# Performance work log

Hardware: AMD Instinct MI355X
Metric: run time of the kernel (lower is better)

## Reference

```python
import jax, jax.numpy as jnp
import numpy as np

B, D, N, H = 1024, 1024, 51, 10
NUM_ITERS = 5
BN_EPS = 1e-3  # Keras BatchNormalization default epsilon


def setup_inputs():
    key = jax.random.key(0)
    ks = jax.random.split(key, 20)
    rn = lambda k, sh, s=0.05: jax.random.normal(k, sh, dtype=jnp.float32) * s
    z = lambda sh: jnp.zeros(sh, jnp.float32)
    o = lambda sh: jnp.ones(sh, jnp.float32)
    return {
        "nonvis_vec": rn(ks[0], (B, 2 * D), 1.0),
        "featuremap": rn(ks[1], (B, H, H, D), 1.0),
        "prior": rn(ks[2], (B, N), 1.0),
        "W1": rn(ks[3], (3 * D, 2 * D)), "b1": z((2 * D,)),
        "g1": o((2 * D,)), "be1": z((2 * D,)), "m1": rn(ks[4], (2 * D,)), "v1": o((2 * D,)),
        "W2": rn(ks[5], (2 * D, D)), "b2": z((D,)),
        "g2": o((D,)), "be2": z((D,)), "m2": rn(ks[6], (D,)), "v2": o((D,)),
        "Wk": rn(ks[7], (D, 3 * D)), "Uk": rn(ks[8], (D, 3 * D)),
        "bi": z((3 * D,)), "br": z((3 * D,)),
        "ct1_w": rn(ks[9], (3, 3, D, D // 4)), "ct1_b": z((D // 4,)),
        "ct2_w": rn(ks[10], (3, 3, D // 4, D // 16)), "ct2_b": z((D // 16,)),
        "ct3_w": rn(ks[11], (3, 3, D // 16, D // 64)), "ct3_b": z((D // 64,)),
        "ct4_w": rn(ks[12], (3, 3, D // 64, 1)), "ct4_b": z((1,)),
        "Ws": rn(ks[13], (3 * D, N)), "bs": z((N,)),
    }


def _bn(x, g, be, m, v):
    # inference-mode batchnorm (moving statistics)
    return (x - m) * jax.lax.rsqrt(v + BN_EPS) * g + be


def _gru_step(x, h, Wk, Uk, bi, br):
    # Keras GRU, reset_after=True, single timestep
    mx = x @ Wk + bi          # [B, 3D]
    mi = h @ Uk + br          # [B, 3D]
    xz, xr, xh = jnp.split(mx, 3, axis=-1)
    iz, ir, ih = jnp.split(mi, 3, axis=-1)
    zg = jax.nn.sigmoid(xz + iz)
    rg = jax.nn.sigmoid(xr + ir)
    hh = jnp.tanh(xh + rg * ih)
    return zg * h + (1.0 - zg) * hh


def _convT(x, w, b):
    return jax.lax.conv_transpose(x, w, (2, 2), 'SAME',
                                  dimension_numbers=('NHWC', 'HWIO', 'NHWC')) + b


def _attention(h, ct1_w, ct1_b, ct2_w, ct2_b, ct3_w, ct3_b, ct4_w, ct4_b):
    b = h.shape[0]
    a = h[:, None, None, :]                                  # [B,1,1,D]
    a = jax.nn.relu(_convT(a, ct1_w, ct1_b))                 # [B,2,2,D/4]
    a = jax.nn.relu(_convT(a, ct2_w, ct2_b))                 # [B,4,4,D/16]
    a = jax.nn.relu(_convT(a, ct3_w, ct3_b))                 # [B,8,8,D/64]
    a = _convT(a, ct4_w, ct4_b)                              # [B,16,16,1]
    a = jax.image.resize(a, (b, H, H, 1), method='bilinear')  # [B,10,10,1]
    # joint softmax over both spatial axes
    a = jax.nn.softmax(a.reshape(b, H * H, 1), axis=1).reshape(b, H, H, 1)
    return a


def reference(nonvis_vec, featuremap, prior, W1, b1, g1, be1, m1, v1,
              W2, b2, g2, be2, m2, v2, Wk, Uk, bi, br,
              ct1_w, ct1_b, ct2_w, ct2_b, ct3_w, ct3_b, ct4_w, ct4_b, Ws, bs):
    vis_vec = jnp.mean(featuremap, axis=(1, 2))              # GlobalAvgPool2D
    combined = jnp.concatenate([nonvis_vec, vis_vec], axis=-1)
    score = combined @ Ws + bs
    h = jnp.zeros((combined.shape[0], D), combined.dtype)
    for _ in range(NUM_ITERS):
        x = _bn(jax.nn.relu(combined @ W1 + b1), g1, be1, m1, v1)
        x = _bn(jax.nn.relu(x @ W2 + b2), g2, be2, m2, v2)
        h = _gru_step(x, h, Wk, Uk, bi, br)
        attn = _attention(h, ct1_w, ct1_b, ct2_w, ct2_b, ct3_w, ct3_b, ct4_w, ct4_b)
        vis_vec = jnp.sum(featuremap * attn, axis=(1, 2))    # attention pooling
        combined = jnp.concatenate([nonvis_vec, vis_vec], axis=-1)
        score = score + combined @ Ws + bs
    score = score / (NUM_ITERS + 1)
    return score + prior
```

## Files before the change

### kernel.cpp

```cpp
#include <hip/hip_runtime.h>

typedef unsigned short u16;
typedef __attribute__((ext_vector_type(8))) __bf16 bf16x8;
typedef __attribute__((ext_vector_type(4))) float f32x4;

typedef __attribute__((address_space(1))) const void gvoid_t;
typedef __attribute__((address_space(3))) void lvoid_t;

enum { E_CADD = 1, E_BIAS = 2, E_RELU = 4, E_AFF = 8, E_WBF = 16, E_WF32 = 32 };

static __device__ __forceinline__ u16 f2bf(float f) {
  unsigned u = __float_as_uint(f);
  u += 0x7fffu + ((u >> 16) & 1u);
  return (u16)(u >> 16);
}
static __device__ __forceinline__ float bf2f(u16 h) {
  return __uint_as_float(((unsigned)h) << 16);
}

template <int FLAGS>
static __device__ __forceinline__ void gemm64_body(
    u16* As, u16* Bs,
    const u16* __restrict__ A, const u16* __restrict__ Bt,
    float* __restrict__ Cf, u16* __restrict__ Cb,
    const float* __restrict__ Cadd, const float* __restrict__ bias,
    const float* __restrict__ scale, const float* __restrict__ shift,
    int N, int K, int bx, int by) {
  const int tid = threadIdx.x;
  const int wave = tid >> 6, lane = tid & 63;
  const int bm = by << 6, bn = bx << 6;
  const int wm = (wave >> 1) << 5, wn = (wave & 1) << 5;
  const int lr = lane & 15, lg = lane >> 4;
  const int rx = lr & 7;

  f32x4 acc[2][2] = {};

  for (int kt = 0; kt < K; kt += 64) {
#pragma unroll
    for (int i = 0; i < 2; ++i) {
      const int li = i * 256 + tid;
      const int row = li >> 3;
      const int cg = (li & 7) ^ (row & 7);
      const int lb = (i * 256 + wave * 64) * 8;
      __builtin_amdgcn_global_load_lds(
          (gvoid_t*)(A + (size_t)(bm + row) * K + kt + (cg << 3)),
          (lvoid_t*)(As + lb), 16, 0, 0);
      __builtin_amdgcn_global_load_lds(
          (gvoid_t*)(Bt + (size_t)(bn + row) * K + kt + (cg << 3)),
          (lvoid_t*)(Bs + lb), 16, 0, 0);
    }
    __syncthreads();
#pragma unroll
    for (int kk = 0; kk < 64; kk += 32) {
      bf16x8 av[2], bv[2];
#pragma unroll
      for (int mi = 0; mi < 2; ++mi)
        av[mi] = *(const bf16x8*)(As + ((wm + mi * 16 + lr) << 6) +
                                  ((((kk >> 3) + lg) ^ rx) << 3));
#pragma unroll
      for (int ni = 0; ni < 2; ++ni)
        bv[ni] = *(const bf16x8*)(Bs + ((wn + ni * 16 + lr) << 6) +
                                  ((((kk >> 3) + lg) ^ rx) << 3));
#pragma unroll
      for (int mi = 0; mi < 2; ++mi)
#pragma unroll
        for (int ni = 0; ni < 2; ++ni)
          acc[mi][ni] = __builtin_amdgcn_mfma_f32_16x16x32_bf16(av[mi], bv[ni], acc[mi][ni], 0, 0, 0);
    }
    __syncthreads();
  }

#pragma unroll
  for (int mi = 0; mi < 2; ++mi) {
#pragma unroll
    for (int ni = 0; ni < 2; ++ni) {
      const int col = bn + wn + ni * 16 + lr;
#pragma unroll
      for (int r = 0; r < 4; ++r) {
        const int row = bm + wm + mi * 16 + (lg << 2) + r;
        float v = acc[mi][ni][r];
        if (FLAGS & E_CADD) v += Cadd[(size_t)row * N + col];
        if (FLAGS & E_BIAS) v += bias[col];
        if (FLAGS & E_RELU) v = fmaxf(v, 0.f);
        if (FLAGS & E_AFF) v = v * scale[col] + shift[col];
        if (FLAGS & E_WF32) Cf[(size_t)row * N + col] = v;
        if (FLAGS & E_WBF) Cb[(size_t)row * N + col] = f2bf(v);
      }
    }
  }
}

template <int FLAGS>
__global__ __launch_bounds__(256) void gemm64_k(
    const u16* __restrict__ A, const u16* __restrict__ Bt,
    float* __restrict__ Cf, u16* __restrict__ Cb,
    const float* __restrict__ Cadd, const float* __restrict__ bias,
    const float* __restrict__ scale, const float* __restrict__ shift,
    int N, int K) {
  __shared__ u16 As[4096], Bs[4096];
  gemm64_body<FLAGS>(As, Bs, A, Bt, Cf, Cb, Cadd, bias, scale, shift, N, K,
                     blockIdx.x, blockIdx.y);
}

template <int F0, int F1>
__global__ __launch_bounds__(256) void gemm64_pair_k(
    const u16* A0, const u16* B0, float* Cf0, u16* Cb0, const float* Cadd0,
    const float* bias0, const float* scale0, const float* shift0, int N0, int K0, int xt0,
    const u16* A1, const u16* B1, float* Cf1, u16* Cb1, const float* Cadd1,
    const float* bias1, const float* scale1, const float* shift1, int N1, int K1, int xt1) {
  __shared__ u16 As[4096], Bs[4096];
  if (blockIdx.z == 0) {
    if ((int)blockIdx.x < xt0)
      gemm64_body<F0>(As, Bs, A0, B0, Cf0, Cb0, Cadd0, bias0, scale0, shift0,
                      N0, K0, blockIdx.x, blockIdx.y);
  } else {
    if ((int)blockIdx.x < xt1)
      gemm64_body<F1>(As, Bs, A1, B1, Cf1, Cb1, Cadd1, bias1, scale1, shift1,
                      N1, K1, blockIdx.x, blockIdx.y);
  }
}

__global__ __launch_bounds__(256) void prep_w_k(
    const float* __restrict__ W1, const float* __restrict__ W2,
    const float* __restrict__ Wk, const float* __restrict__ Uk,
    const float* __restrict__ Ws,
    u16* __restrict__ W1nv_t, u16* __restrict__ W1v_t, u16* __restrict__ W2t,
    u16* __restrict__ Wkt, u16* __restrict__ Ukt,
    u16* __restrict__ Wsnv_t, u16* __restrict__ Wsv_t) {
  int b = blockIdx.x;
  const float* in; u16* out; int ld, k0, K, Nv, kT;
  if (b < 1024)      {           in = W1; out = W1nv_t; ld = 2048; k0 = 0;    K = 2048; Nv = 2048; kT = 32; }
  else if (b < 1536) { b -= 1024; in = W1; out = W1v_t;  ld = 2048; k0 = 2048; K = 1024; Nv = 2048; kT = 16; }
  else if (b < 2048) { b -= 1536; in = W2; out = W2t;   ld = 1024; k0 = 0;    K = 2048; Nv = 1024; kT = 32; }
  else if (b < 2816) { b -= 2048; in = Wk; out = Wkt;   ld = 3072; k0 = 0;    K = 1024; Nv = 3072; kT = 16; }
  else if (b < 3584) { b -= 2816; in = Uk; out = Ukt;   ld = 3072; k0 = 0;    K = 1024; Nv = 3072; kT = 16; }
  else if (b < 3648) { b -= 3584; in = Ws; out = Wsnv_t; ld = 51;  k0 = 0;    K = 2048; Nv = 51;   kT = 32; }
  else               { b -= 3648; in = Ws; out = Wsv_t;  ld = 51;  k0 = 2048; K = 1024; Nv = 51;   kT = 16; }
  const int kt = (b % kT) << 6, nt = (b / kT) << 6;
  __shared__ float t[64][65];
  const int tx = threadIdx.x & 63, ty = threadIdx.x >> 6;
#pragma unroll
  for (int i = 0; i < 16; ++i) {
    const int kl = ty + i * 4;
    const int n = nt + tx;
    t[kl][tx] = (n < Nv) ? in[(size_t)(k0 + kt + kl) * ld + n] : 0.f;
  }
  __syncthreads();
#pragma unroll
  for (int i = 0; i < 16; ++i)
    out[(size_t)(nt + ty + i * 4) * K + kt + tx] = f2bf(t[tx][ty + i * 4]);
}

__global__ void build_all_k(
    const float* __restrict__ w1, const float* __restrict__ b1c,
    const float* __restrict__ w2, const float* __restrict__ b2c,
    const float* __restrict__ w3, const float* __restrict__ b3c,
    const float* __restrict__ w4, const float* __restrict__ b4c,
    u16* __restrict__ Wp1, u16* __restrict__ Wp2,
    u16* __restrict__ Wp3, u16* __restrict__ Wp4,
    float* __restrict__ bp1, float* __restrict__ bp2,
    float* __restrict__ bp3, float* __restrict__ bp4) {
  int y = blockIdx.y;
  const float* w; const float* bin; u16* wp; float* bp; int Si, CI, CO, n;
  if (y < 1024)      { n = y;        w = w1; bin = b1c; wp = Wp1; bp = bp1; Si = 1; CI = 1024; CO = 256; }
  else if (y < 2048) { n = y - 1024; w = w2; bin = b2c; wp = Wp2; bp = bp2; Si = 2; CI = 256;  CO = 64; }
  else if (y < 3072) { n = y - 2048; w = w3; bin = b3c; wp = Wp3; bp = bp3; Si = 4; CI = 64;   CO = 16; }
  else               { n = y - 3072; w = w4; bin = b4c; wp = Wp4; bp = bp4; Si = 8; CI = 16;   CO = 1; }
  const int So = Si * 2;
  const int K = Si * Si * CI;
  const int k = blockIdx.x * 256 + threadIdx.x;
  const int co = n % CO;
  const int pox = (n / CO) % So;
  const int poy = n / (CO * So);
  const int ci = k % CI;
  const int pix = (k / CI) % Si;
  const int piy = k / (CI * Si);
  int wy = -1, wx = -1;
  if (poy & 1) { if (piy == (poy >> 1)) wy = 1; }
  else { if (piy == (poy >> 1)) wy = 2; else if (piy == (poy >> 1) - 1) wy = 0; }
  if (pox & 1) { if (pix == (pox >> 1)) wx = 1; }
  else { if (pix == (pox >> 1)) wx = 2; else if (pix == (pox >> 1) - 1) wx = 0; }
  float v = 0.f;
  if (wy >= 0 && wx >= 0) v = w[((size_t)(wy * 3 + wx) * CI + ci) * CO + co];
  wp[(size_t)n * K + k] = f2bf(v);
  if (k == 0) bp[n] = bin[co];
}

__global__ __launch_bounds__(256) void fm_pass_k(
    const float* __restrict__ fm, u16* __restrict__ fmb,
    float* __restrict__ vis_sum, u16* __restrict__ visb, int wfmb) {
  const int b = blockIdx.x;
  const int d0 = threadIdx.x << 2;
  const float* p = fm + (size_t)b * 102400 + d0;
  float s0 = 0, s1 = 0, s2 = 0, s3 = 0;
  for (int pp = 0; pp < 100; ++pp) {
    const float4 v = *(const float4*)(p + pp * 1024);
    if (wfmb) {
      ushort4 u;
      u.x = f2bf(v.x); u.y = f2bf(v.y); u.z = f2bf(v.z); u.w = f2bf(v.w);
      *(ushort4*)(fmb + (size_t)b * 102400 + pp * 1024 + d0) = u;
    }
    s0 += v.x; s1 += v.y; s2 += v.z; s3 += v.w;
  }
  const float inv = 1.0f / 100.0f;
  s0 *= inv; s1 *= inv; s2 *= inv; s3 *= inv;
  const int o = (b << 10) + d0;
  float4 m; m.x = s0; m.y = s1; m.z = s2; m.w = s3;
  *(float4*)(vis_sum + o) = m;
  ushort4 u; u.x = f2bf(s0); u.y = f2bf(s1); u.z = f2bf(s2); u.w = f2bf(s3);
  *(ushort4*)(visb + o) = u;
}

__global__ __launch_bounds__(256) void misc_k(
    const float* __restrict__ nonvis, u16* __restrict__ nonvis_b,
    const float* g1, const float* be1, const float* m1, const float* v1,
    const float* g2, const float* be2, const float* m2, const float* v2,
    const float* bs, float* scale1, float* shift1, float* scale2, float* shift2,
    float* bs_pad, float* __restrict__ hf, u16* __restrict__ hb) {
  const int i = blockIdx.x * 256 + threadIdx.x;
  if (i < 2097152) nonvis_b[i] = f2bf(nonvis[i]);
  if (i < 1048576) { hf[i] = 0.f; hb[i] = 0; }
  if (i < 2048) { float sc = g1[i] * rsqrtf(v1[i] + 1e-3f); scale1[i] = sc; shift1[i] = be1[i] - m1[i] * sc; }
  if (i < 1024) { float sc = g2[i] * rsqrtf(v2[i] + 1e-3f); scale2[i] = sc; shift2[i] = be2[i] - m2[i] * sc; }
  if (i < 128) bs_pad[i] = (i < 51) ? bs[i] : 0.f;
}

__global__ __launch_bounds__(256) void gru_k(const float* __restrict__ mx, const float* __restrict__ mi,
                                             float* __restrict__ hf, u16* __restrict__ hb) {
  const int idx = blockIdx.x * 256 + threadIdx.x;
  const int b = idx >> 10, d = idx & 1023;
  const float* mxb = mx + (size_t)b * 3072;
  const float* mib = mi + (size_t)b * 3072;
  const float xz = mxb[d], xr = mxb[d + 1024], xh = mxb[d + 2048];
  const float iz = mib[d], ir = mib[d + 1024], ih = mib[d + 2048];
  const float zg = 1.f / (1.f + expf(-(xz + iz)));
  const float rg = 1.f / (1.f + expf(-(xr + ir)));
  const float hh = tanhf(xh + rg * ih);
  const float hn = zg * hf[idx] + (1.f - zg) * hh;
  hf[idx] = hn;
  hb[idx] = f2bf(hn);
}

static __device__ __forceinline__ void taps(int o, int& si, float* w) {
  const float s = 1.6f * (float)o + 0.3f;
  int s0 = (int)ceilf(s - 1.6f);
  if (s0 < 0) s0 = 0;
  si = s0;
  float sum = 0.f;
#pragma unroll
  for (int j = 0; j < 4; ++j) {
    const int i = s0 + j;
    float ww = 0.f;
    if (i <= 15) {
      const float d = fabsf(s - (float)i) * (1.0f / 1.6f);
      ww = fmaxf(0.f, 1.f - d);
    }
    w[j] = ww;
    sum += ww;
  }
  const float inv = 1.f / sum;
#pragma unroll
  for (int j = 0; j < 4; ++j) w[j] *= inv;
}

__global__ __launch_bounds__(128) void attn_k(const float* __restrict__ a4, float* __restrict__ attn) {
  const int b = blockIdx.x, t = threadIdx.x;
  __shared__ float sm[128];
  float val = -1e30f;
  if (t < 100) {
    const int oy = t / 10, ox = t - oy * 10;
    int siy, six;
    float wy[4], wx[4];
    taps(oy, siy, wy);
    taps(ox, six, wx);
    const float* p = a4 + (b << 8);
    float s = 0.f;
#pragma unroll
    for (int jy = 0; jy < 4; ++jy) {
      const int iy = min(siy + jy, 15);
      float rs = 0.f;
#pragma unroll
      for (int jx = 0; jx < 4; ++jx) {
        const int ix = min(six + jx, 15);
        rs += wx[jx] * p[(iy << 4) + ix];
      }
      s += wy[jy] * rs;
    }
    val = s;
  }
  sm[t] = val;
  __syncthreads();
  for (int off = 64; off > 0; off >>= 1) {
    if (t < off) sm[t] = fmaxf(sm[t], sm[t + off]);
    __syncthreads();
  }
  const float mx = sm[0];
  __syncthreads();
  const float e = (t < 100) ? expf(val - mx) : 0.f;
  sm[t] = e;
  __syncthreads();
  for (int off = 64; off > 0; off >>= 1) {
    if (t < off) sm[t] += sm[t + off];
    __syncthreads();
  }
  if (t < 100) attn[b * 100 + t] = e / sm[0];
}

__global__ __launch_bounds__(256) void wsum_bf16_k(const u16* __restrict__ fmb,
                                                   const float* __restrict__ attn,
                                                   float* __restrict__ vis_sum,
                                                   u16* __restrict__ visb,
                                                   u16* __restrict__ vsb) {
  const int b = blockIdx.x;
  __shared__ float at[100];
  if (threadIdx.x < 100) at[threadIdx.x] = attn[b * 100 + threadIdx.x];
  __syncthreads();
  const int d0 = threadIdx.x << 2;
  const u16* p = fmb + (size_t)b * 102400 + d0;
  float s0 = 0, s1 = 0, s2 = 0, s3 = 0;
  for (int pp = 0; pp < 100; ++pp) {
    const ushort4 v = *(const ushort4*)(p + pp * 1024);
    const float a = at[pp];
    s0 += a * bf2f(v.x); s1 += a * bf2f(v.y); s2 += a * bf2f(v.z); s3 += a * bf2f(v.w);
  }
  const int o = (b << 10) + d0;
  float4 vs = *(float4*)(vis_sum + o);
  vs.x += s0; vs.y += s1; vs.z += s2; vs.w += s3;
  *(float4*)(vis_sum + o) = vs;
  ushort4 u; u.x = f2bf(s0); u.y = f2bf(s1); u.z = f2bf(s2); u.w = f2bf(s3);
  *(ushort4*)(visb + o) = u;
  ushort4 w; w.x = f2bf(vs.x); w.y = f2bf(vs.y); w.z = f2bf(vs.z); w.w = f2bf(vs.w);
  *(ushort4*)(vsb + o) = w;
}

__global__ __launch_bounds__(256) void wsum_f32_k(const float* __restrict__ fm,
                                                  const float* __restrict__ attn,
                                                  float* __restrict__ vis_sum,
                                                  u16* __restrict__ visb,
                                                  u16* __restrict__ vsb) {
  const int b = blockIdx.x;
  __shared__ float at[100];
  if (threadIdx.x < 100) at[threadIdx.x] = attn[b * 100 + threadIdx.x];
  __syncthreads();
  const int d0 = threadIdx.x << 2;
  const float* p = fm + (size_t)b * 102400 + d0;
  float s0 = 0, s1 = 0, s2 = 0, s3 = 0;
  for (int pp = 0; pp < 100; ++pp) {
    const float4 v = *(const float4*)(p + pp * 1024);
    const float a = at[pp];
    s0 += a * v.x; s1 += a * v.y; s2 += a * v.z; s3 += a * v.w;
  }
  const int o = (b << 10) + d0;
  float4 vs = *(float4*)(vis_sum + o);
  vs.x += s0; vs.y += s1; vs.z += s2; vs.w += s3;
  *(float4*)(vis_sum + o) = vs;
  ushort4 u; u.x = f2bf(s0); u.y = f2bf(s1); u.z = f2bf(s2); u.w = f2bf(s3);
  *(ushort4*)(visb + o) = u;
  ushort4 w; w.x = f2bf(vs.x); w.y = f2bf(vs.y); w.z = f2bf(vs.z); w.w = f2bf(vs.w);
  *(ushort4*)(vsb + o) = w;
}

__global__ void final_k(const float* __restrict__ V, const float* __restrict__ snv,
                        const float* __restrict__ prior, float* __restrict__ out) {
  const int idx = blockIdx.x * 256 + threadIdx.x;
  if (idx >= 1024 * 51) return;
  const int b = idx / 51, n = idx - b * 51;
  out[idx] = V[(b << 7) + n] * (1.f / 6.f) + snv[(b << 7) + n] + prior[idx];
}

extern "C" void kernel_launch(void* const* d_in, const int* in_sizes, int n_in,
                              void* d_out, int out_size, void* d_ws, size_t ws_size,
                              hipStream_t stream) {
  (void)in_sizes; (void)n_in; (void)out_size;
  const float* nonvis = (const float*)d_in[0];
  const float* fm     = (const float*)d_in[1];
  const float* prior  = (const float*)d_in[2];
  const float* W1     = (const float*)d_in[3];
  const float* b1     = (const float*)d_in[4];
  const float* g1     = (const float*)d_in[5];
  const float* be1    = (const float*)d_in[6];
  const float* m1     = (const float*)d_in[7];
  const float* v1     = (const float*)d_in[8];
  const float* W2     = (const float*)d_in[9];
  const float* b2     = (const float*)d_in[10];
  const float* g2     = (const float*)d_in[11];
  const float* be2    = (const float*)d_in[12];
  const float* m2     = (const float*)d_in[13];
  const float* v2     = (const float*)d_in[14];
  const float* Wk     = (const float*)d_in[15];
  const float* Uk     = (const float*)d_in[16];
  const float* bi     = (const float*)d_in[17];
  const float* br     = (const float*)d_in[18];
  const float* ct1w   = (const float*)d_in[19];
  const float* ct1b   = (const float*)d_in[20];
  const float* ct2w   = (const float*)d_in[21];
  const float* ct2b   = (const float*)d_in[22];
  const float* ct3w   = (const float*)d_in[23];
  const float* ct3b   = (const float*)d_in[24];
  const float* ct4w   = (const float*)d_in[25];
  const float* ct4b   = (const float*)d_in[26];
  const float* Ws     = (const float*)d_in[27];
  const float* bs     = (const float*)d_in[28];

  char* base = (char*)d_ws;
  size_t off = 0;
  auto alloc = [&](size_t bytes) -> void* {
    void* r = base + off;
    off = (off + bytes + 255) & ~(size_t)255;
    return r;
  };

  u16* nonvis_b = (u16*)alloc(4194304);
  u16* W1nv_t   = (u16*)alloc(8388608);
  u16* W1v_t    = (u16*)alloc(4194304);
  u16* W2t      = (u16*)alloc(4194304);
  u16* Wkt      = (u16*)alloc(6291456);
  u16* Ukt      = (u16*)alloc(6291456);
  u16* Wsnv_t   = (u16*)alloc(524288);
  u16* Wsv_t    = (u16*)alloc(262144);
  u16* Wp1      = (u16*)alloc(2097152);
  u16* Wp2      = (u16*)alloc(2097152);
  u16* Wp3      = (u16*)alloc(2097152);
  u16* Wp4      = (u16*)alloc(524288);
  float* bp1    = (float*)alloc(4096);
  float* bp2    = (float*)alloc(4096);
  float* bp3    = (float*)alloc(4096);
  float* bp4    = (float*)alloc(1024);
  float* scale1 = (float*)alloc(8192);
  float* shift1 = (float*)alloc(8192);
  float* scale2 = (float*)alloc(4096);
  float* shift2 = (float*)alloc(4096);
  float* bs_pad = (float*)alloc(512);
  float* P1     = (float*)alloc(8388608);
  float* snv    = (float*)alloc(524288);
  u16* x1       = (u16*)alloc(4194304);
  u16* x2       = (u16*)alloc(2097152);
  float* mx     = (float*)alloc(12582912);
  float* mi     = (float*)alloc(12582912);
  float* hf     = (float*)alloc(4194304);
  u16* hb       = (u16*)alloc(2097152);
  u16* a1       = (u16*)alloc(2097152);
  u16* a2       = (u16*)alloc(2097152);
  u16* a3       = (u16*)alloc(2097152);
  float* a4     = (float*)alloc(1048576);
  float* attn   = (float*)alloc(409600);
  float* vis_sum= (float*)alloc(4194304);
  u16* visb     = (u16*)alloc(2097152);
  u16* vsb      = (u16*)alloc(2097152);
  float* V      = (float*)alloc(524288);
  u16* fmb = nullptr;
  int use_fmb = 0;
  if (off + (size_t)209715200 + 256 <= ws_size) {
    fmb = (u16*)alloc(209715200);
    use_fmb = 1;
  }

  misc_k<<<8192, 256, 0, stream>>>(nonvis, nonvis_b, g1, be1, m1, v1, g2, be2, m2, v2,
                                   bs, scale1, shift1, scale2, shift2, bs_pad, hf, hb);
  prep_w_k<<<3680, 256, 0, stream>>>(W1, W2, Wk, Uk, Ws,
                                     W1nv_t, W1v_t, W2t, Wkt, Ukt, Wsnv_t, Wsv_t);
  build_all_k<<<dim3(4, 3328), 256, 0, stream>>>(ct1w, ct1b, ct2w, ct2b, ct3w, ct3b, ct4w, ct4b,
                                                 Wp1, Wp2, Wp3, Wp4, bp1, bp2, bp3, bp4);
  fm_pass_k<<<1024, 256, 0, stream>>>(fm, fmb, vis_sum, visb, use_fmb);

  gemm64_pair_k<E_BIAS | E_WF32, E_BIAS | E_WF32><<<dim3(32, 16, 2), 256, 0, stream>>>(
      nonvis_b, W1nv_t, P1, nullptr, nullptr, b1, nullptr, nullptr, 2048, 2048, 32,
      nonvis_b, Wsnv_t, snv, nullptr, nullptr, bs_pad, nullptr, nullptr, 128, 2048, 2);

  for (int it = 0; it < 5; ++it) {
    gemm64_pair_k<E_CADD | E_RELU | E_AFF | E_WBF, E_BIAS | E_WF32>
        <<<dim3(48, 16, 2), 256, 0, stream>>>(
        visb, W1v_t, nullptr, x1, P1, nullptr, scale1, shift1, 2048, 1024, 32,
        hb, Ukt, mi, nullptr, nullptr, br, nullptr, nullptr, 3072, 1024, 48);
    gemm64_k<E_BIAS | E_RELU | E_AFF | E_WBF><<<dim3(16, 16), 256, 0, stream>>>(
        x1, W2t, nullptr, x2, nullptr, b2, scale2, shift2, 1024, 2048);
    gemm64_k<E_BIAS | E_WF32><<<dim3(48, 16), 256, 0, stream>>>(
        x2, Wkt, mx, nullptr, nullptr, bi, nullptr, nullptr, 3072, 1024);
    gru_k<<<4096, 256, 0, stream>>>(mx, mi, hf, hb);
    gemm64_k<E_BIAS | E_RELU | E_WBF><<<dim3(16, 16), 256, 0, stream>>>(
        hb, Wp1, nullptr, a1, nullptr, bp1, nullptr, nullptr, 1024, 1024);
    gemm64_k<E_BIAS | E_RELU | E_WBF><<<dim3(16, 16), 256, 0, stream>>>(
        a1, Wp2, nullptr, a2, nullptr, bp2, nullptr, nullptr, 1024, 1024);
    gemm64_k<E_BIAS | E_RELU | E_WBF><<<dim3(16, 16), 256, 0, stream>>>(
        a2, Wp3, nullptr, a3, nullptr, bp3, nullptr, nullptr, 1024, 1024);
    gemm64_k<E_BIAS | E_WF32><<<dim3(4, 16), 256, 0, stream>>>(
        a3, Wp4, a4, nullptr, nullptr, bp4, nullptr, nullptr, 256, 1024);
    attn_k<<<1024, 128, 0, stream>>>(a4, attn);
    if (use_fmb)
      wsum_bf16_k<<<1024, 256, 0, stream>>>(fmb, attn, vis_sum, visb, vsb);
    else
      wsum_f32_k<<<1024, 256, 0, stream>>>(fm, attn, vis_sum, visb, vsb);
  }

  gemm64_k<E_WF32><<<dim3(2, 16), 256, 0, stream>>>(
      vsb, Wsv_t, V, nullptr, nullptr, nullptr, nullptr, nullptr, 128, 1024);
  final_k<<<204, 256, 0, stream>>>(V, snv, prior, (float*)d_out);
}
```

Baseline: 1.150 ms.

## Double-buffer GEMM LDS staging and widen N tiles to 128 with 512 threads

Generalizes the bf16 MFMA GEMM to a templated N-tile width (64 or 128) with 8 waves per block. LDS is double-buffered so the next K-tile's global→LDS load is issued before computing on the current one, with one barrier per K step instead of two. The wide N=2048/3072 GEMMs use 128-wide tiles, giving more reuse of A loads and fewer blocks. The trade-off is doubled LDS use, which may lower occupancy, and a smaller per-wave M slice on the 64-wide variant.

```diff
diff --git a/kernel.cpp b/kernel.cpp
--- a/kernel.cpp
+++ b/kernel.cpp
@@ -18,8 +18,8 @@
   return __uint_as_float(((unsigned)h) << 16);
 }
 
-template <int FLAGS>
-static __device__ __forceinline__ void gemm64_body(
+template <int FLAGS, int BN>
+static __device__ __forceinline__ void gemmX_body(
     u16* As, u16* Bs,
     const u16* __restrict__ A, const u16* __restrict__ Bt,
     float* __restrict__ Cf, u16* __restrict__ Cb,
@@ -28,50 +28,64 @@
     int N, int K, int bx, int by) {
   const int tid = threadIdx.x;
   const int wave = tid >> 6, lane = tid & 63;
-  const int bm = by << 6, bn = bx << 6;
-  const int wm = (wave >> 1) << 5, wn = (wave & 1) << 5;
+  const int bm = by << 6, bn = bx * BN;
   const int lr = lane & 15, lg = lane >> 4;
   const int rx = lr & 7;
-
-  f32x4 acc[2][2] = {};
-
-  for (int kt = 0; kt < K; kt += 64) {
-#pragma unroll
-    for (int i = 0; i < 2; ++i) {
-      const int li = i * 256 + tid;
+  const int wm = (BN == 64) ? ((wave >> 1) << 4) : ((wave >> 2) << 5);
+  const int wn = (BN == 64) ? ((wave & 1) << 5) : ((wave & 3) << 5);
+  constexpr int MI = (BN == 64) ? 1 : 2;
+  constexpr int NB = BN / 64;
+
+  f32x4 acc[MI][2] = {};
+
+  auto stage = [&](int buf, int kt) {
+    {
+      const int row = tid >> 3;
+      const int cg = (tid & 7) ^ (row & 7);
+      __builtin_amdgcn_global_load_lds(
+          (gvoid_t*)(A + (size_t)(bm + row) * K + kt + (cg << 3)),
+          (lvoid_t*)(As + buf * 4096 + wave * 512), 16, 0, 0);
+    }
+#pragma unroll
+    for (int i = 0; i < NB; ++i) {
+      const int li = i * 512 + tid;
       const int row = li >> 3;
       const int cg = (li & 7) ^ (row & 7);
-      const int lb = (i * 256 + wave * 64) * 8;
-      __builtin_amdgcn_global_load_lds(
-          (gvoid_t*)(A + (size_t)(bm + row) * K + kt + (cg << 3)),
-          (lvoid_t*)(As + lb), 16, 0, 0);
       __builtin_amdgcn_global_load_lds(
           (gvoid_t*)(Bt + (size_t)(bn + row) * K + kt + (cg << 3)),
-          (lvoid_t*)(Bs + lb), 16, 0, 0);
-    }
+          (lvoid_t*)(Bs + buf * (BN * 64) + i * 4096 + wave * 512), 16, 0, 0);
+    }
+  };
+
+  stage(0, 0);
+  int buf = 0;
+  for (int kt = 0; kt < K; kt += 64) {
     __syncthreads();
+    if (kt + 64 < K) stage(buf ^ 1, kt + 64);
+    const u16* Ab = As + buf * 4096;
+    const u16* Bb = Bs + buf * (BN * 64);
 #pragma unroll
     for (int kk = 0; kk < 64; kk += 32) {
-      bf16x8 av[2], bv[2];
-#pragma unroll
-      for (int mi = 0; mi < 2; ++mi)
-        av[mi] = *(const bf16x8*)(As + ((wm + mi * 16 + lr) << 6) +
+      bf16x8 av[MI], bv[2];
+#pragma unroll
+      for (int mi = 0; mi < MI; ++mi)
+        av[mi] = *(const bf16x8*)(Ab + ((wm + mi * 16 + lr) << 6) +
                                   ((((kk >> 3) + lg) ^ rx) << 3));
 #pragma unroll
       for (int ni = 0; ni < 2; ++ni)
-        bv[ni] = *(const bf16x8*)(Bs + ((wn + ni * 16 + lr) << 6) +
+        bv[ni] = *(const bf16x8*)(Bb + ((wn + ni * 16 + lr) << 6) +
                                   ((((kk >> 3) + lg) ^ rx) << 3));
 #pragma unroll
-      for (int mi = 0; mi < 2; ++mi)
+      for (int mi = 0; mi < MI; ++mi)
 #pragma unroll
         for (int ni = 0; ni < 2; ++ni)
           acc[mi][ni] = __builtin_amdgcn_mfma_f32_16x16x32_bf16(av[mi], bv[ni], acc[mi][ni], 0, 0, 0);
     }
-    __syncthreads();
-  }
-
-#pragma unroll
-  for (int mi = 0; mi < 2; ++mi) {
+    buf ^= 1;
+  }
+
+#pragma unroll
+  for (int mi = 0; mi < MI; ++mi) {
 #pragma unroll
     for (int ni = 0; ni < 2; ++ni) {
       const int col = bn + wn + ni * 16 + lr;
@@ -90,33 +104,36 @@
   }
 }
 
-template <int FLAGS>
-__global__ __launch_bounds__(256) void gemm64_k(
+template <int FLAGS, int BN>
+__global__ __launch_bounds__(512) void gemmX_k(
     const u16* __restrict__ A, const u16* __restrict__ Bt,
     float* __restrict__ Cf, u16* __restrict__ Cb,
     const float* __restrict__ Cadd, const float* __restrict__ bias,
     const float* __restrict__ scale, const float* __restrict__ shift,
     int N, int K) {
-  __shared__ u16 As[4096], Bs[4096];
-  gemm64_body<FLAGS>(As, Bs, A, Bt, Cf, Cb, Cadd, bias, scale, shift, N, K,
-                     blockIdx.x, blockIdx.y);
-}
-
-template <int F0, int F1>
-__global__ __launch_bounds__(256) void gemm64_pair_k(
+  __shared__ u16 As[2 * 4096];
+  __shared__ u16 Bs[2 * BN * 64];
+  gemmX_body<FLAGS, BN>(As, Bs, A, Bt, Cf, Cb, Cadd, bias, scale, shift, N, K,
+                        blockIdx.x, blockIdx.y);
+}
+
+template <int F0, int BN0, int F1, int BN1>
+__global__ __launch_bounds__(512) void gemmX_pair_k(
     const u16* A0, const u16* B0, float* Cf0, u16* Cb0, const float* Cadd0,
     const float* bias0, const float* scale0, const float* shift0, int N0, int K0, int xt0,
     const u16* A1, const u16* B1, float* Cf1, u16* Cb1, const float* Cadd1,
     const float* bias1, const float* scale1, const float* shift1, int N1, int K1, int xt1) {
-  __shared__ u16 As[4096], Bs[4096];
+  constexpr int BMAX = (BN0 > BN1) ? BN0 : BN1;
+  __shared__ u16 As[2 * 4096];
+  __shared__ u16 Bs[2 * BMAX * 64];
   if (blockIdx.z == 0) {
     if ((int)blockIdx.x < xt0)
-      gemm64_body<F0>(As, Bs, A0, B0, Cf0, Cb0, Cadd0, bias0, scale0, shift0,
-                      N0, K0, blockIdx.x, blockIdx.y);
+      gemmX_body<F0, BN0>(As, Bs, A0, B0, Cf0, Cb0, Cadd0, bias0, scale0, shift0,
+                          N0, K0, blockIdx.x, blockIdx.y);
   } else {
     if ((int)blockIdx.x < xt1)
-      gemm64_body<F1>(As, Bs, A1, B1, Cf1, Cb1, Cadd1, bias1, scale1, shift1,
-                      N1, K1, blockIdx.x, blockIdx.y);
+      gemmX_body<F1, BN1>(As, Bs, A1, B1, Cf1, Cb1, Cadd1, bias1, scale1, shift1,
+                          N1, K1, blockIdx.x, blockIdx.y);
   }
 }
 
@@ -463,27 +480,27 @@
                                                  Wp1, Wp2, Wp3, Wp4, bp1, bp2, bp3, bp4);
   fm_pass_k<<<1024, 256, 0, stream>>>(fm, fmb, vis_sum, visb, use_fmb);
 
-  gemm64_pair_k<E_BIAS | E_WF32, E_BIAS | E_WF32><<<dim3(32, 16, 2), 256, 0, stream>>>(
-      nonvis_b, W1nv_t, P1, nullptr, nullptr, b1, nullptr, nullptr, 2048, 2048, 32,
-      nonvis_b, Wsnv_t, snv, nullptr, nullptr, bs_pad, nullptr, nullptr, 128, 2048, 2);
+  gemmX_pair_k<E_BIAS | E_WF32, 128, E_BIAS | E_WF32, 128><<<dim3(16, 16, 2), 512, 0, stream>>>(
+      nonvis_b, W1nv_t, P1, nullptr, nullptr, b1, nullptr, nullptr, 2048, 2048, 16,
+      nonvis_b, Wsnv_t, snv, nullptr, nullptr, bs_pad, nullptr, nullptr, 128, 2048, 1);
 
   for (int it = 0; it < 5; ++it) {
-    gemm64_pair_k<E_CADD | E_RELU | E_AFF | E_WBF, E_BIAS | E_WF32>
-        <<<dim3(48, 16, 2), 256, 0, stream>>>(
-        visb, W1v_t, nullptr, x1, P1, nullptr, scale1, shift1, 2048, 1024, 32,
-        hb, Ukt, mi, nullptr, nullptr, br, nullptr, nullptr, 3072, 1024, 48);
-    gemm64_k<E_BIAS | E_RELU | E_AFF | E_WBF><<<dim3(16, 16), 256, 0, stream>>>(
+    gemmX_pair_k<E_CADD | E_RELU | E_AFF | E_WBF, 128, E_BIAS | E_WF32, 128>
+        <<<dim3(24, 16, 2), 512, 0, stream>>>(
+        visb, W1v_t, nullptr, x1, P1, nullptr, scale1, shift1, 2048, 1024, 16,
+        hb, Ukt, mi, nullptr, nullptr, br, nullptr, nullptr, 3072, 1024, 24);
+    gemmX_k<E_BIAS | E_RELU | E_AFF | E_WBF, 64><<<dim3(16, 16), 512, 0, stream>>>(
         x1, W2t, nullptr, x2, nullptr, b2, scale2, shift2, 1024, 2048);
-    gemm64_k<E_BIAS | E_WF32><<<dim3(48, 16), 256, 0, stream>>>(
+    gemmX_k<E_BIAS | E_WF32, 128><<<dim3(24, 16), 512, 0, stream>>>(
         x2, Wkt, mx, nullptr, nullptr, bi, nullptr, nullptr, 3072, 1024);
     gru_k<<<4096, 256, 0, stream>>>(mx, mi, hf, hb);
-    gemm64_k<E_BIAS | E_RELU | E_WBF><<<dim3(16, 16), 256, 0, stream>>>(
+    gemmX_k<E_BIAS | E_RELU | E_WBF, 64><<<dim3(16, 16), 512, 0, stream>>>(
         hb, Wp1, nullptr, a1, nullptr, bp1, nullptr, nullptr, 1024, 1024);
-    gemm64_k<E_BIAS | E_RELU | E_WBF><<<dim3(16, 16), 256, 0, stream>>>(
+    gemmX_k<E_BIAS | E_RELU | E_WBF, 64><<<dim3(16, 16), 512, 0, stream>>>(
         a1, Wp2, nullptr, a2, nullptr, bp2, nullptr, nullptr, 1024, 1024);
-    gemm64_k<E_BIAS | E_RELU | E_WBF><<<dim3(16, 16), 256, 0, stream>>>(
+    gemmX_k<E_BIAS | E_RELU | E_WBF, 64><<<dim3(16, 16), 512, 0, stream>>>(
         a2, Wp3, nullptr, a3, nullptr, bp3, nullptr, nullptr, 1024, 1024);
-    gemm64_k<E_BIAS | E_WF32><<<dim3(4, 16), 256, 0, stream>>>(
+    gemmX_k<E_BIAS | E_WF32, 64><<<dim3(4, 16), 512, 0, stream>>>(
         a3, Wp4, a4, nullptr, nullptr, bp4, nullptr, nullptr, 256, 1024);
     attn_k<<<1024, 128, 0, stream>>>(a4, attn);
     if (use_fmb)
@@ -492,7 +509,7 @@
       wsum_f32_k<<<1024, 256, 0, stream>>>(fm, attn, vis_sum, visb, vsb);
   }
 
-  gemm64_k<E_WF32><<<dim3(2, 16), 256, 0, stream>>>(
+  gemmX_k<E_WF32, 128><<<dim3(1, 16), 512, 0, stream>>>(
       vsb, Wsv_t, V, nullptr, nullptr, nullptr, nullptr, nullptr, 128, 1024);
   final_k<<<204, 256, 0, stream>>>(V, snv, prior, (float*)d_out);
 }
```

After: 1.116 ms. -3.0%, faster.
